# Optimization experiments

Measured on AMD Instinct MI355X. Metric: run time of the kernel, lower is better.

Reference implementation:

```python
import jax, jax.numpy as jnp
import numpy as np
from math import sqrt

D_MODEL = 1024
N_HEADS = 16
D_T = 256
D_HID = 4 * D_MODEL
EPS = 1e-6


def _rmsnorm(x):
    # RMSNorm without affine: x / sqrt(mean(x^2) + eps)
    return x * jax.lax.rsqrt(jnp.mean(x * x, axis=-1, keepdims=True) + EPS)


def setup_inputs() -> dict:
    key = jax.random.key(0)
    ks = jax.random.split(key, 16)
    s = 0.02  # weight init scale
    inp = {
        "x": jax.random.normal(ks[0], (4, 2048, D_MODEL), dtype=jnp.float32),
        "t": jax.random.normal(ks[1], (4, D_T), dtype=jnp.float32),
        # AdaRMSNorm (attn) : Linear(d_t, d_model, bias=False) weights stored (out, in)
        "attn_gamma_w": jax.random.normal(ks[2], (D_MODEL, D_T), dtype=jnp.float32) * s,
        "attn_beta_w": jax.random.normal(ks[3], (D_MODEL, D_T), dtype=jnp.float32) * s,
        # Attention projections
        "W_q": jax.random.normal(ks[4], (D_MODEL, D_MODEL), dtype=jnp.float32) * s,
        "W_k": jax.random.normal(ks[5], (D_MODEL, D_MODEL), dtype=jnp.float32) * s,
        "W_v": jax.random.normal(ks[6], (D_MODEL, D_MODEL), dtype=jnp.float32) * s,
        "W_o": jax.random.normal(ks[7], (D_MODEL, D_MODEL), dtype=jnp.float32) * s,
        "attn_alpha_w": jax.random.normal(ks[8], (D_MODEL, D_T), dtype=jnp.float32) * s,
        # AdaRMSNorm (ffn)
        "ffn_gamma_w": jax.random.normal(ks[9], (D_MODEL, D_T), dtype=jnp.float32) * s,
        "ffn_beta_w": jax.random.normal(ks[10], (D_MODEL, D_T), dtype=jnp.float32) * s,
        # SwiGLU
        "gate_w": jax.random.normal(ks[11], (D_HID, D_MODEL), dtype=jnp.float32) * s,
        "hidden_w": jax.random.normal(ks[12], (D_HID, D_MODEL), dtype=jnp.float32) * s,
        "out_w": jax.random.normal(ks[13], (D_MODEL, D_HID), dtype=jnp.float32) * s,
        "out_b": jnp.zeros((D_MODEL,), dtype=jnp.float32),
        "ffn_alpha_w": jax.random.normal(ks[14], (D_MODEL, D_T), dtype=jnp.float32) * s,
    }
    return inp


def _ada_rmsnorm(x, t, gamma_w, beta_w):
    gamma = (t @ gamma_w.T)[:, None, :]  # [b, 1, d]
    beta = (t @ beta_w.T)[:, None, :]
    return gamma * _rmsnorm(x) + beta


def _attention(x, W_q, W_k, W_v, W_o):
    b, l, dm = x.shape
    d_head = dm // N_HEADS
    scale = sqrt(N_HEADS / dm)  # == 1/sqrt(d_head)
    def split(y):  # [b, l, dm] -> [b, n, l, d]
        return y.reshape(b, l, N_HEADS, d_head).transpose(0, 2, 1, 3)
    q = split(x @ W_q.T)
    k = split(x @ W_k.T)
    v = split(x @ W_v.T)
    attn = jax.nn.softmax(scale * jnp.einsum("bnqd,bnkd->bnqk", q, k), axis=-1)
    o = jnp.einsum("bnqk,bnkd->bnqd", attn, v)
    o = o.transpose(0, 2, 1, 3).reshape(b, l, dm)
    return o @ W_o.T


def _swiglu(x, gate_w, hidden_w, out_w, out_b):
    return (jax.nn.silu(x @ gate_w.T) * (x @ hidden_w.T)) @ out_w.T + out_b


def reference(x, t, attn_gamma_w, attn_beta_w, W_q, W_k, W_v, W_o, attn_alpha_w,
              ffn_gamma_w, ffn_beta_w, gate_w, hidden_w, out_w, out_b, ffn_alpha_w):
    a_alpha = (t @ attn_alpha_w.T)[:, None, :]
    x = x + a_alpha * _attention(_ada_rmsnorm(x, t, attn_gamma_w, attn_beta_w), W_q, W_k, W_v, W_o)
    f_alpha = (t @ ffn_alpha_w.T)[:, None, :]
    return x + f_alpha * _swiglu(_ada_rmsnorm(x, t, ffn_gamma_w, ffn_beta_w), gate_w, hidden_w, out_w, out_b)
```

## Files before the change

kernel.cpp:

```cpp
#include <hip/hip_runtime.h>
#include <hip/hip_bf16.h>

typedef __attribute__((ext_vector_type(8))) short short8;
typedef __attribute__((ext_vector_type(4))) short short4v;
typedef __attribute__((ext_vector_type(4))) float f32x4;
using bf16 = __hip_bfloat16;
using lds_bf16 = __attribute__((address_space(3))) bf16;

#define BARF()  asm volatile("s_barrier" ::: "memory")
#define LGKM0() asm volatile("s_waitcnt lgkmcnt(0)" ::: "memory")
#define VMC4()  asm volatile("s_waitcnt vmcnt(4)" ::: "memory")
#define VMC0()  asm volatile("s_waitcnt vmcnt(0)" ::: "memory")
#define SCHED0() __builtin_amdgcn_sched_barrier(0)
#define PRIO1() __builtin_amdgcn_s_setprio(1)
#define PRIO0() __builtin_amdgcn_s_setprio(0)

static __device__ __forceinline__ short bfb(float f) {
  bf16 h = __float2bfloat16(f);
  short r; __builtin_memcpy(&r, &h, 2); return r;
}

static __device__ __forceinline__ void gld_lds16(const bf16* g, bf16* l) {
  __builtin_amdgcn_global_load_lds(
      (const __attribute__((address_space(1))) void*)g,
      (__attribute__((address_space(3))) void*)l, 16, 0, 0);
}

static __device__ __forceinline__ short8 dsr(const lds_bf16* b, int imm) {
  short8 v;
  asm volatile("ds_read_b128 %0, %1 offset:%2" : "=v"(v) : "v"(b), "i"(imm));
  return v;
}

__global__ __launch_bounds__(256) void cvt_all_kernel(
    const float* __restrict__ s0, const float* __restrict__ s1, const float* __restrict__ s2,
    const float* __restrict__ s3, const float* __restrict__ gw, const float* __restrict__ hw,
    const float* __restrict__ ow, bf16* __restrict__ dbase) {
  size_t c = (size_t)blockIdx.x * 256 + threadIdx.x;
  const float* src; size_t se;
  if (c < 524288) {
    int seg = (int)(c >> 17);
    src = (seg == 0) ? s0 : (seg == 1) ? s1 : (seg == 2) ? s2 : s3;
    se = (c - ((size_t)seg << 17)) * 8;
  } else if (c < 1572864) {
    size_t lc = c - 524288;
    size_t row = lc >> 7;
    src = (row & 1) ? hw : gw;
    se = ((row >> 1) << 10) + ((lc & 127) << 3);
  } else { src = ow; se = (c - 1572864) * 8; }
  float4 v0 = *(const float4*)(src + se);
  float4 v1 = *(const float4*)(src + se + 4);
  short8 o;
  o[0] = bfb(v0.x); o[1] = bfb(v0.y); o[2] = bfb(v0.z); o[3] = bfb(v0.w);
  o[4] = bfb(v1.x); o[5] = bfb(v1.y); o[6] = bfb(v1.z); o[7] = bfb(v1.w);
  *(short8*)(dbase + c * 8) = o;
}

__global__ __launch_bounds__(256) void tproj_kernel(const float* __restrict__ t,
    const float* __restrict__ w0, const float* __restrict__ w1, const float* __restrict__ w2,
    const float* __restrict__ w3, const float* __restrict__ w4, const float* __restrict__ w5,
    float* __restrict__ out) {
  int gid = blockIdx.x * 256 + threadIdx.x;
  int s = gid >> 12, rem = gid & 4095;
  int b = rem >> 10, n = rem & 1023;
  const float* w = (s == 0) ? w0 : (s == 1) ? w1 : (s == 2) ? w2 : (s == 3) ? w3 : (s == 4) ? w4 : w5;
  const float4* tv = (const float4*)(t + b * 256);
  const float4* wv = (const float4*)(w + n * 256);
  float acc = 0.f;
  #pragma unroll 8
  for (int j = 0; j < 64; ++j) {
    float4 a = tv[j], c = wv[j];
    acc += a.x * c.x + a.y * c.y + a.z * c.z + a.w * c.w;
  }
  out[gid] = acc;
}

__global__ __launch_bounds__(256) void ada_rms_kernel(const float* __restrict__ x,
    const float* __restrict__ gamma, const float* __restrict__ beta, bf16* __restrict__ out) {
  int row = blockIdx.x;
  int b = row >> 11;
  int tid = threadIdx.x;
  const float* xr = x + (size_t)row * 1024;
  float4 v = *(const float4*)(xr + tid * 4);
  float ss = v.x * v.x + v.y * v.y + v.z * v.z + v.w * v.w;
  #pragma unroll
  for (int m = 1; m < 64; m <<= 1) ss += __shfl_xor(ss, m);
  __shared__ float red[4];
  if ((tid & 63) == 0) red[tid >> 6] = ss;
  __syncthreads();
  float tot = red[0] + red[1] + red[2] + red[3];
  float rinv = rsqrtf(tot * (1.0f / 1024.0f) + 1e-6f);
  const float* g  = gamma + b * 1024 + tid * 4;
  const float* be = beta  + b * 1024 + tid * 4;
  short4v o;
  o[0] = bfb(g[0] * v.x * rinv + be[0]);
  o[1] = bfb(g[1] * v.y * rinv + be[1]);
  o[2] = bfb(g[2] * v.z * rinv + be[2]);
  o[3] = bfb(g[3] * v.w * rinv + be[3]);
  *(short4v*)(out + (size_t)row * 1024 + tid * 4) = o;
}

enum { EPI8_GH = 1 };

#define RDA_M(d, mh) { \
  _Pragma("unroll") for (int mq = 0; mq < 4; ++mq) { \
    a[mq][0] = dsr(aB0, (d) * 32768 + ((mh) * 4 + mq) * 2048); \
    a[mq][1] = dsr(aB1, (d) * 32768 + ((mh) * 4 + mq) * 2048); } }
#define RDB0_M(d, nh) { \
  _Pragma("unroll") for (int nq = 0; nq < 2; ++nq) { \
    b0[nq][0] = dsr(bB0, (d) * 32768 + ((nh) * 2 + nq) * 2048); \
    b0[nq][1] = dsr(bB1, (d) * 32768 + ((nh) * 2 + nq) * 2048); } }
#define RDB1_M(d, nh) { \
  _Pragma("unroll") for (int nq = 0; nq < 2; ++nq) { \
    b1[nq][0] = dsr(bB0, (d) * 32768 + ((nh) * 2 + nq) * 2048); \
    b1[nq][1] = dsr(bB1, (d) * 32768 + ((nh) * 2 + nq) * 2048); } }

template<int EPI>
__global__ __launch_bounds__(512, 2) void gemm8p_kernel(
    const bf16* __restrict__ A, const bf16* __restrict__ B,
    int N, int K,
    bf16* __restrict__ o1)
{
  __shared__ __align__(16) bf16 sA[2 * 2 * 128 * 64];
  __shared__ __align__(16) bf16 sB[2 * 2 * 128 * 64];
  const int tid = threadIdx.x;
  const int lane = tid & 63, w = tid >> 6;
  const int wr = w >> 2, wcn = w & 3;
  const int bid = (int)blockIdx.x;
  const int ntn = N >> 8;
  const int trow = (bid / ntn) << 8;
  const int tcol = (bid % ntn) << 8;
  const int fr = lane & 15, hi = lane >> 4;
  const int rbase = hi << 2;
  const int NITER = K >> 7;
  const int st_row = (w << 4) + (lane >> 3);
  const int st_col = (((lane & 7) ^ ((lane >> 3) & 7)) << 3);
  const bf16* AsH0 = A + (size_t)(trow + st_row) * K + st_col;
  const bf16* AsH1 = AsH0 + (size_t)128 * K;
  const bf16* BsH0 = B + (size_t)(tcol + st_row) * K + st_col;
  const bf16* BsH1 = BsH0 + (size_t)128 * K;
  const size_t K8 = (size_t)K << 3;
  bf16* dA = sA + (w << 10);
  bf16* dB = sB + (w << 10);

  auto stA = [&](int dbuf, int h, int t) {
    const bf16* s = (h ? AsH1 : AsH0) + (t << 6);
    bf16* d = dA + ((dbuf * 2 + h) << 13);
    gld_lds16(s, d);
    gld_lds16(s + K8, d + 512);
  };
  auto stB = [&](int dbuf, int h, int t) {
    const bf16* s = (h ? BsH1 : BsH0) + (t << 6);
    bf16* d = dB + ((dbuf * 2 + h) << 13);
    gld_lds16(s, d);
    gld_lds16(s + K8, d + 512);
  };
  const int colK0 = (hi << 3) ^ ((fr & 7) << 3);
  const int colK1 = (32 + (hi << 3)) ^ ((fr & 7) << 3);
  const lds_bf16* aB0 = (const lds_bf16*)(sA + (wr << 13) + (fr << 6) + colK0);
  const lds_bf16* aB1 = (const lds_bf16*)(sA + (wr << 13) + (fr << 6) + colK1);
  const lds_bf16* bB0 = (const lds_bf16*)(sB + ((wcn >> 1) << 13) + ((wcn & 1) << 12) + (fr << 6) + colK0);
  const lds_bf16* bB1 = (const lds_bf16*)(sB + ((wcn >> 1) << 13) + ((wcn & 1) << 12) + (fr << 6) + colK1);

  f32x4 acc[8][4] = {};
  short8 a[4][2], b0[2][2], b1[2][2];

  auto QUAD0 = [&](int mh, int nh) {
    #pragma unroll
    for (int kk = 0; kk < 2; ++kk)
      #pragma unroll
      for (int mq = 0; mq < 4; ++mq)
        #pragma unroll
        for (int nq = 0; nq < 2; ++nq)
          acc[mh * 4 + mq][nh * 2 + nq] = __builtin_amdgcn_mfma_f32_16x16x32_bf16(
              a[mq][kk], b0[nq][kk], acc[mh * 4 + mq][nh * 2 + nq], 0, 0, 0);
  };
  auto QUAD1 = [&](int mh, int nh) {
    #pragma unroll
    for (int kk = 0; kk < 2; ++kk)
      #pragma unroll
      for (int mq = 0; mq < 4; ++mq)
        #pragma unroll
        for (int nq = 0; nq < 2; ++nq)
          acc[mh * 4 + mq][nh * 2 + nq] = __builtin_amdgcn_mfma_f32_16x16x32_bf16(
              a[mq][kk], b1[nq][kk], acc[mh * 4 + mq][nh * 2 + nq], 0, 0, 0);
  };

  stB(0, 0, 0); stB(0, 1, 0); stA(0, 0, 0); stA(0, 1, 0);
  stB(1, 0, 1); stB(1, 1, 1);
  VMC4();
  BARF();

  for (int i = 0; i < NITER; ++i) {
    const int t1 = 2 * i + 1, tn0 = 2 * i + 2, tn1 = 2 * i + 3;
    const bool g = (i != NITER - 1);
    RDA_M(0, 0); RDB0_M(0, 0);
    stA(1, 0, t1);
    BARF(); LGKM0(); SCHED0(); PRIO1(); QUAD0(0, 0); PRIO0(); BARF();
    RDB1_M(0, 1);
    stA(1, 1, t1);
    BARF(); LGKM0(); SCHED0(); PRIO1(); QUAD1(0, 1); PRIO0(); BARF();
    RDA_M(0, 1);
    if (g) stB(0, 0, tn0);
    BARF(); LGKM0(); SCHED0(); PRIO1(); QUAD1(1, 1); PRIO0(); BARF();
    if (g) stB(0, 1, tn0);
    BARF(); LGKM0(); SCHED0(); PRIO1(); QUAD0(1, 0); PRIO0();
    if (g) { VMC4(); } else { VMC0(); }
    BARF();
    RDA_M(1, 0); RDB0_M(1, 0);
    if (g) stA(0, 0, tn0);
    BARF(); LGKM0(); SCHED0(); PRIO1(); QUAD0(0, 0); PRIO0(); BARF();
    RDB1_M(1, 1);
    if (g) stA(0, 1, tn0);
    BARF(); LGKM0(); SCHED0(); PRIO1(); QUAD1(0, 1); PRIO0(); BARF();
    RDA_M(1, 1);
    if (g) stB(1, 0, tn1);
    BARF(); LGKM0(); SCHED0(); PRIO1(); QUAD1(1, 1); PRIO0(); BARF();
    if (g) stB(1, 1, tn1);
    BARF(); LGKM0(); SCHED0(); PRIO1(); QUAD0(1, 0); PRIO0();
    if (g) { VMC4(); }
    BARF();
  }

  #pragma unroll
  for (int m = 0; m < 8; ++m)
  #pragma unroll
  for (int n = 0; n < 4; ++n)
  #pragma unroll
  for (int r = 0; r < 4; ++r) {
    int row = trow + (wr << 7) + m * 16 + rbase + r;
    int col = tcol + (wcn << 6) + n * 16 + fr;
    float c = acc[m][n][r];
    float other = __shfl_xor(c, 1);
    if (!(fr & 1)) {
      float sg = c / (1.f + __expf(-c));
      o1[(size_t)row * 4096 + (col >> 1)] = __float2bfloat16(sg * other);
    }
  }
}

enum { EPI_RESID = 0, EPI_FINAL = 1, EPI_QKV3 = 2 };

template<int EPI>
__global__ __launch_bounds__(256) void gemm_bt_kernel(
    const bf16* __restrict__ A, const bf16* __restrict__ B,
    int N, int K,
    float* __restrict__ outF,
    const float* __restrict__ aux1, const float* __restrict__ aux2,
    const float* __restrict__ bias,
    bf16* __restrict__ oq, bf16* __restrict__ okk, bf16* __restrict__ ovt)
{
  __shared__ __align__(16) bf16 As[128][32];
  __shared__ __align__(16) bf16 Bs[128][32];
  const int tid = threadIdx.x;
  const int lane = tid & 63, wid = tid >> 6;
  const int wr = wid >> 1, wc = wid & 1;
  const int bid = (int)blockIdx.x;
  const int ntn = N >> 7;
  const int trow = (bid / ntn) << 7;
  const int tcol = (bid % ntn) << 7;
  const int fr = lane & 15, fc = (lane >> 4) << 3;
  const int rbase = (lane >> 4) << 2;
  const bf16* gA0 = A + (size_t)(trow + wid * 32 + (lane >> 2)) * K + ((lane & 3) << 3);
  const bf16* gA1 = gA0 + (size_t)16 * K;
  const bf16* gB0 = B + (size_t)(tcol + wid * 32 + (lane >> 2)) * K + ((lane & 3) << 3);
  const bf16* gB1 = gB0 + (size_t)16 * K;
  bf16* lA0 = &As[wid * 32][0];
  bf16* lA1 = &As[wid * 32 + 16][0];
  bf16* lB0 = &Bs[wid * 32][0];
  bf16* lB1 = &Bs[wid * 32 + 16][0];
  f32x4 acc[4][4] = {};
  for (int k0 = 0; k0 < K; k0 += 32) {
    __syncthreads();
    gld_lds16(gA0 + k0, lA0);
    gld_lds16(gA1 + k0, lA1);
    gld_lds16(gB0 + k0, lB0);
    gld_lds16(gB1 + k0, lB1);
    __syncthreads();
    short8 af[4], bfr[4];
    #pragma unroll
    for (int m = 0; m < 4; ++m) af[m] = *(const short8*)&As[wr * 64 + m * 16 + fr][fc];
    #pragma unroll
    for (int n = 0; n < 4; ++n) bfr[n] = *(const short8*)&Bs[wc * 64 + n * 16 + fr][fc];
    #pragma unroll
    for (int m = 0; m < 4; ++m)
      #pragma unroll
      for (int n = 0; n < 4; ++n)
        acc[m][n] = __builtin_amdgcn_mfma_f32_16x16x32_bf16(af[m], bfr[n], acc[m][n], 0, 0, 0);
  }
  if constexpr (EPI == EPI_QKV3) {
    #pragma unroll
    for (int m = 0; m < 4; ++m)
    #pragma unroll
    for (int n = 0; n < 4; ++n) {
      int row0 = trow + wr * 64 + m * 16 + rbase;
      int col  = tcol + wc * 64 + n * 16 + fr;
      int seg = col >> 10, cc = col & 1023;
      int bb = row0 >> 11, h2 = cc >> 6, dd = cc & 63;
      if (seg == 0) {
        #pragma unroll
        for (int r = 0; r < 4; ++r) {
          int l = (row0 + r) & 2047;
          oq[(((size_t)(bb * 16 + h2) * 2048 + l) << 6) + dd] =
              __float2bfloat16(acc[m][n][r] * 0.18033688f);
        }
      } else if (seg == 1) {
        #pragma unroll
        for (int r = 0; r < 4; ++r) {
          int l = (row0 + r) & 2047;
          okk[(((size_t)(bb * 16 + h2) * 2048 + l) << 6) + dd] = __float2bfloat16(acc[m][n][r]);
        }
      } else {
        int l = row0 & 2047;
        short4v o4;
        #pragma unroll
        for (int r = 0; r < 4; ++r) o4[r] = bfb(acc[m][n][r]);
        *(short4v*)&ovt[(((size_t)(bb * 16 + h2) * 64 + dd) << 11) + l] = o4;
      }
    }
  } else {
    #pragma unroll
    for (int m = 0; m < 4; ++m)
    #pragma unroll
    for (int n = 0; n < 4; ++n)
    #pragma unroll
    for (int r = 0; r < 4; ++r) {
      int row = trow + wr * 64 + m * 16 + rbase + r;
      int col = tcol + wc * 64 + n * 16 + fr;
      float c = acc[m][n][r];
      int b = row >> 11;
      size_t idx = (size_t)row * 1024 + col;
      if constexpr (EPI == EPI_RESID) {
        outF[idx] = aux1[idx] + aux2[b * 1024 + col] * c;
      } else {
        outF[idx] = aux1[idx] + aux2[b * 1024 + col] * (c + bias[col]);
      }
    }
  }
}

__global__ __launch_bounds__(512, 4) void attn_kernel(const bf16* __restrict__ q,
    const bf16* __restrict__ k, const bf16* __restrict__ vt, bf16* __restrict__ o) {
  const int id = blockIdx.x;
  const int bh = id & 63;
  const int qt = id >> 6;
  const int b = bh >> 4, h = bh & 15;
  __shared__ __align__(16) bf16 Ks[2][64][72];
  __shared__ __align__(16) bf16 Vs[2][64][72];
  __shared__ __align__(16) bf16 Ps[256][72];
  const int tid = threadIdx.x, lane = tid & 63, w = tid >> 6;
  const int fr = lane & 15, hi = lane >> 4;
  const int fc = hi << 3, rbase = hi << 2;
  const bf16* qbase = q + ((size_t)bh * 2048 + qt * 256) * 64;
  const bf16* kbase = k + (size_t)bh * 2048 * 64;
  const bf16* vbase = vt + (size_t)bh * 64 * 2048;
  short8 qf[2][2];
  #pragma unroll
  for (int nq = 0; nq < 2; ++nq)
    #pragma unroll
    for (int ks = 0; ks < 2; ++ks)
      qf[nq][ks] = *(const short8*)(qbase + (size_t)(w * 32 + nq * 16 + fr) * 64 + ks * 32 + fc);
  short8 onesf;
  #pragma unroll
  for (int j = 0; j < 8; ++j) onesf[j] = (short)0x3F80;
  f32x4 accO[4][2] = {};
  f32x4 accD[2] = {};
  const int sr = tid >> 3, sc = (tid & 7) << 3;
  *(short8*)&Ks[0][sr][sc] = *(const short8*)(kbase + (size_t)sr * 64 + sc);
  *(short8*)&Vs[0][sr][sc] = *(const short8*)(vbase + (size_t)sr * 2048 + sc);
  short8 rk = *(const short8*)(kbase + (size_t)(64 + sr) * 64 + sc);
  short8 rv = *(const short8*)(vbase + (size_t)sr * 2048 + 64 + sc);
  __syncthreads();
  for (int kt = 0; kt < 2048; kt += 64) {
    const int cur = (kt >> 6) & 1;
    if (kt + 64 < 2048) {
      *(short8*)&Ks[cur ^ 1][sr][sc] = rk;
      *(short8*)&Vs[cur ^ 1][sr][sc] = rv;
      if (kt + 128 < 2048) {
        rk = *(const short8*)(kbase + (size_t)(kt + 128 + sr) * 64 + sc);
        rv = *(const short8*)(vbase + (size_t)sr * 2048 + kt + 128 + sc);
      }
    }
    f32x4 s[4][2] = {};
    #pragma unroll
    for (int ks = 0; ks < 2; ++ks) {
      short8 kf[4];
      #pragma unroll
      for (int mk = 0; mk < 4; ++mk) kf[mk] = *(const short8*)&Ks[cur][mk * 16 + fr][ks * 32 + fc];
      #pragma unroll
      for (int mk = 0; mk < 4; ++mk)
        #pragma unroll
        for (int nq = 0; nq < 2; ++nq)
          s[mk][nq] = __builtin_amdgcn_mfma_f32_16x16x32_bf16(kf[mk], qf[nq][ks], s[mk][nq], 0, 0, 0);
    }
    #pragma unroll
    for (int mk = 0; mk < 4; ++mk)
      #pragma unroll
      for (int nq = 0; nq < 2; ++nq) {
        short4v pk;
        pk[0] = bfb(exp2f(s[mk][nq][0]));
        pk[1] = bfb(exp2f(s[mk][nq][1]));
        pk[2] = bfb(exp2f(s[mk][nq][2]));
        pk[3] = bfb(exp2f(s[mk][nq][3]));
        *(short4v*)&Ps[w * 32 + nq * 16 + fr][mk * 16 + rbase] = pk;
      }
    #pragma unroll
    for (int ks2 = 0; ks2 < 2; ++ks2) {
      short8 av[4], bp[2];
      #pragma unroll
      for (int nd = 0; nd < 4; ++nd) av[nd] = *(const short8*)&Vs[cur][nd * 16 + fr][ks2 * 32 + fc];
      #pragma unroll
      for (int nq = 0; nq < 2; ++nq) bp[nq] = *(const short8*)&Ps[w * 32 + nq * 16 + fr][ks2 * 32 + fc];
      #pragma unroll
      for (int nd = 0; nd < 4; ++nd)
        #pragma unroll
        for (int nq = 0; nq < 2; ++nq)
          accO[nd][nq] = __builtin_amdgcn_mfma_f32_16x16x32_bf16(av[nd], bp[nq], accO[nd][nq], 0, 0, 0);
      #pragma unroll
      for (int nq = 0; nq < 2; ++nq)
        accD[nq] = __builtin_amdgcn_mfma_f32_16x16x32_bf16(onesf, bp[nq], accD[nq], 0, 0, 0);
    }
    __syncthreads();
  }
  float rd[2];
  #pragma unroll
  for (int nq = 0; nq < 2; ++nq) rd[nq] = 1.0f / accD[nq][0];
  #pragma unroll
  for (int nd = 0; nd < 4; ++nd)
    #pragma unroll
    for (int nq = 0; nq < 2; ++nq) {
      short4v ov;
      #pragma unroll
      for (int r = 0; r < 4; ++r) ov[r] = bfb(accO[nd][nq][r] * rd[nq]);
      int qrow = qt * 256 + w * 32 + nq * 16 + fr;
      int col = h * 64 + nd * 16 + rbase;
      *(short4v*)&o[((size_t)b * 2048 + qrow) * 1024 + col] = ov;
    }
}

extern "C" void kernel_launch(void* const* d_in, const int* in_sizes, int n_in,
                              void* d_out, int out_size, void* d_ws, size_t ws_size,
                              hipStream_t stream) {
  (void)in_sizes; (void)n_in; (void)out_size; (void)ws_size;
  const float* x   = (const float*)d_in[0];
  const float* t   = (const float*)d_in[1];
  const float* agw = (const float*)d_in[2];
  const float* abw = (const float*)d_in[3];
  const float* wq  = (const float*)d_in[4];
  const float* wk  = (const float*)d_in[5];
  const float* wv  = (const float*)d_in[6];
  const float* wo  = (const float*)d_in[7];
  const float* aaw = (const float*)d_in[8];
  const float* fgw = (const float*)d_in[9];
  const float* fbw = (const float*)d_in[10];
  const float* gw  = (const float*)d_in[11];
  const float* hw  = (const float*)d_in[12];
  const float* ow  = (const float*)d_in[13];
  const float* ob  = (const float*)d_in[14];
  const float* faw = (const float*)d_in[15];
  float* out = (float*)d_out;

  char* p = (char*)d_ws;
  auto alloc = [&](size_t bytes) -> char* {
    char* r = p; p += (bytes + 255) & ~(size_t)255; return r;
  };
  float* tp    = (float*)alloc((size_t)6 * 4096 * 4);
  bf16* wq_b   = (bf16*)alloc((size_t)1024 * 1024 * 2);
  bf16* wk_b   = (bf16*)alloc((size_t)1024 * 1024 * 2);
  bf16* wv_b   = (bf16*)alloc((size_t)1024 * 1024 * 2);
  bf16* wo_b   = (bf16*)alloc((size_t)1024 * 1024 * 2);
  bf16* wgh_b  = (bf16*)alloc((size_t)8192 * 1024 * 2);
  bf16* wout_b = (bf16*)alloc((size_t)1024 * 4096 * 2);
  bf16* xn_b   = (bf16*)alloc((size_t)8192 * 1024 * 2);
  bf16* q_b    = (bf16*)alloc((size_t)8192 * 1024 * 2);
  bf16* k_b    = (bf16*)alloc((size_t)8192 * 1024 * 2);
  bf16* vt_b   = (bf16*)alloc((size_t)8192 * 1024 * 2);
  bf16* ao_b   = (bf16*)alloc((size_t)8192 * 1024 * 2);
  float* xmid  = (float*)alloc((size_t)8192 * 1024 * 4);
  bf16* gh_b   = (bf16*)alloc((size_t)8192 * 4096 * 2);

  cvt_all_kernel<<<8192, 256, 0, stream>>>(wq, wk, wv, wo, gw, hw, ow, wq_b);
  tproj_kernel<<<96, 256, 0, stream>>>(t, agw, abw, aaw, fgw, fbw, faw, tp);
  ada_rms_kernel<<<8192, 256, 0, stream>>>(x, tp + 0 * 4096, tp + 1 * 4096, xn_b);
  gemm_bt_kernel<EPI_QKV3><<<1536, 256, 0, stream>>>(xn_b, wq_b, 3072, 1024,
      nullptr, nullptr, nullptr, nullptr, q_b, k_b, vt_b);
  attn_kernel<<<512, 512, 0, stream>>>(q_b, k_b, vt_b, ao_b);
  gemm_bt_kernel<EPI_RESID><<<512, 256, 0, stream>>>(ao_b, wo_b, 1024, 1024, xmid, x, tp + 2 * 4096, nullptr, nullptr, nullptr, nullptr);
  ada_rms_kernel<<<8192, 256, 0, stream>>>(xmid, tp + 3 * 4096, tp + 4 * 4096, xn_b);
  gemm8p_kernel<EPI8_GH><<<1024, 512, 0, stream>>>(xn_b, wgh_b, 8192, 1024, gh_b);
  gemm_bt_kernel<EPI_FINAL><<<512, 256, 0, stream>>>(gh_b, wout_b, 1024, 4096, out, xmid, tp + 5 * 4096, ob, nullptr, nullptr, nullptr);
}
```

Baseline: 558.3 us.

## Route FFN down-projection through pipelined 256x128 8-wave GEMM; reorder attention K/V staging

```diff
diff --git a/kernel.cpp b/kernel.cpp
--- a/kernel.cpp
+++ b/kernel.cpp
@@ -10,6 +10,7 @@
 #define BARF()  asm volatile("s_barrier" ::: "memory")
 #define LGKM0() asm volatile("s_waitcnt lgkmcnt(0)" ::: "memory")
 #define VMC4()  asm volatile("s_waitcnt vmcnt(4)" ::: "memory")
+#define VMC2()  asm volatile("s_waitcnt vmcnt(2)" ::: "memory")
 #define VMC0()  asm volatile("s_waitcnt vmcnt(0)" ::: "memory")
 #define SCHED0() __builtin_amdgcn_sched_barrier(0)
 #define PRIO1() __builtin_amdgcn_s_setprio(1)
@@ -100,7 +101,7 @@
   *(short4v*)(out + (size_t)row * 1024 + tid * 4) = o;
 }
 
-enum { EPI8_GH = 1 };
+enum { EPI8_GH = 1, EPI8_FIN = 2 };
 
 #define RDA_M(d, mh) { \
   _Pragma("unroll") for (int mq = 0; mq < 4; ++mq) { \
@@ -114,22 +115,27 @@
   _Pragma("unroll") for (int nq = 0; nq < 2; ++nq) { \
     b1[nq][0] = dsr(bB0, (d) * 32768 + ((nh) * 2 + nq) * 2048); \
     b1[nq][1] = dsr(bB1, (d) * 32768 + ((nh) * 2 + nq) * 2048); } }
-
-template<int EPI>
+#define RDB0_F(d) { b0[0][0] = dsr(bB0, (d) * 16384); b0[0][1] = dsr(bB1, (d) * 16384); }
+#define RDB1_F(d) { b1[0][0] = dsr(bB0, (d) * 16384 + 2048); b1[0][1] = dsr(bB1, (d) * 16384 + 2048); }
+
+template<int EPI, int BN>
 __global__ __launch_bounds__(512, 2) void gemm8p_kernel(
     const bf16* __restrict__ A, const bf16* __restrict__ B,
     int N, int K,
-    bf16* __restrict__ o1)
+    bf16* __restrict__ o1, float* __restrict__ outF,
+    const float* __restrict__ aux1, const float* __restrict__ aux2,
+    const float* __restrict__ bias)
 {
+  constexpr int SB_ELEMS = (BN == 256) ? (2 * 2 * 128 * 64) : (2 * 128 * 64);
   __shared__ __align__(16) bf16 sA[2 * 2 * 128 * 64];
-  __shared__ __align__(16) bf16 sB[2 * 2 * 128 * 64];
+  __shared__ __align__(16) bf16 sB[SB_ELEMS];
   const int tid = threadIdx.x;
   const int lane = tid & 63, w = tid >> 6;
   const int wr = w >> 2, wcn = w & 3;
   const int bid = (int)blockIdx.x;
-  const int ntn = N >> 8;
+  const int ntn = (BN == 256) ? (N >> 8) : (N >> 7);
   const int trow = (bid / ntn) << 8;
-  const int tcol = (bid % ntn) << 8;
+  const int tcol = (bid % ntn) * BN;
   const int fr = lane & 15, hi = lane >> 4;
   const int rbase = hi << 2;
   const int NITER = K >> 7;
@@ -149,9 +155,15 @@
     gld_lds16(s, d);
     gld_lds16(s + K8, d + 512);
   };
-  auto stB = [&](int dbuf, int h, int t) {
+  auto stB2 = [&](int dbuf, int h, int t) {
     const bf16* s = (h ? BsH1 : BsH0) + (t << 6);
     bf16* d = dB + ((dbuf * 2 + h) << 13);
+    gld_lds16(s, d);
+    gld_lds16(s + K8, d + 512);
+  };
+  auto stB1 = [&](int dbuf, int t) {
+    const bf16* s = BsH0 + (t << 6);
+    bf16* d = dB + (dbuf << 13);
     gld_lds16(s, d);
     gld_lds16(s + K8, d + 512);
   };
@@ -159,87 +171,147 @@
   const int colK1 = (32 + (hi << 3)) ^ ((fr & 7) << 3);
   const lds_bf16* aB0 = (const lds_bf16*)(sA + (wr << 13) + (fr << 6) + colK0);
   const lds_bf16* aB1 = (const lds_bf16*)(sA + (wr << 13) + (fr << 6) + colK1);
-  const lds_bf16* bB0 = (const lds_bf16*)(sB + ((wcn >> 1) << 13) + ((wcn & 1) << 12) + (fr << 6) + colK0);
-  const lds_bf16* bB1 = (const lds_bf16*)(sB + ((wcn >> 1) << 13) + ((wcn & 1) << 12) + (fr << 6) + colK1);
-
-  f32x4 acc[8][4] = {};
+  const lds_bf16 *bB0, *bB1;
+  if constexpr (BN == 256) {
+    bB0 = (const lds_bf16*)(sB + ((wcn >> 1) << 13) + ((wcn & 1) << 12) + (fr << 6) + colK0);
+    bB1 = (const lds_bf16*)(sB + ((wcn >> 1) << 13) + ((wcn & 1) << 12) + (fr << 6) + colK1);
+  } else {
+    bB0 = (const lds_bf16*)(sB + (wcn << 11) + (fr << 6) + colK0);
+    bB1 = (const lds_bf16*)(sB + (wcn << 11) + (fr << 6) + colK1);
+  }
+
+  f32x4 acc[8][BN / 64] = {};
   short8 a[4][2], b0[2][2], b1[2][2];
 
-  auto QUAD0 = [&](int mh, int nh) {
-    #pragma unroll
-    for (int kk = 0; kk < 2; ++kk)
-      #pragma unroll
-      for (int mq = 0; mq < 4; ++mq)
-        #pragma unroll
-        for (int nq = 0; nq < 2; ++nq)
-          acc[mh * 4 + mq][nh * 2 + nq] = __builtin_amdgcn_mfma_f32_16x16x32_bf16(
-              a[mq][kk], b0[nq][kk], acc[mh * 4 + mq][nh * 2 + nq], 0, 0, 0);
-  };
-  auto QUAD1 = [&](int mh, int nh) {
-    #pragma unroll
-    for (int kk = 0; kk < 2; ++kk)
-      #pragma unroll
-      for (int mq = 0; mq < 4; ++mq)
-        #pragma unroll
-        for (int nq = 0; nq < 2; ++nq)
-          acc[mh * 4 + mq][nh * 2 + nq] = __builtin_amdgcn_mfma_f32_16x16x32_bf16(
-              a[mq][kk], b1[nq][kk], acc[mh * 4 + mq][nh * 2 + nq], 0, 0, 0);
-  };
-
-  stB(0, 0, 0); stB(0, 1, 0); stA(0, 0, 0); stA(0, 1, 0);
-  stB(1, 0, 1); stB(1, 1, 1);
-  VMC4();
-  BARF();
-
-  for (int i = 0; i < NITER; ++i) {
-    const int t1 = 2 * i + 1, tn0 = 2 * i + 2, tn1 = 2 * i + 3;
-    const bool g = (i != NITER - 1);
-    RDA_M(0, 0); RDB0_M(0, 0);
-    stA(1, 0, t1);
-    BARF(); LGKM0(); SCHED0(); PRIO1(); QUAD0(0, 0); PRIO0(); BARF();
-    RDB1_M(0, 1);
-    stA(1, 1, t1);
-    BARF(); LGKM0(); SCHED0(); PRIO1(); QUAD1(0, 1); PRIO0(); BARF();
-    RDA_M(0, 1);
-    if (g) stB(0, 0, tn0);
-    BARF(); LGKM0(); SCHED0(); PRIO1(); QUAD1(1, 1); PRIO0(); BARF();
-    if (g) stB(0, 1, tn0);
-    BARF(); LGKM0(); SCHED0(); PRIO1(); QUAD0(1, 0); PRIO0();
-    if (g) { VMC4(); } else { VMC0(); }
+  if constexpr (BN == 256) {
+    auto QUAD0 = [&](int mh, int nh) {
+      #pragma unroll
+      for (int kk = 0; kk < 2; ++kk)
+        #pragma unroll
+        for (int mq = 0; mq < 4; ++mq)
+          #pragma unroll
+          for (int nq = 0; nq < 2; ++nq)
+            acc[mh * 4 + mq][nh * 2 + nq] = __builtin_amdgcn_mfma_f32_16x16x32_bf16(
+                a[mq][kk], b0[nq][kk], acc[mh * 4 + mq][nh * 2 + nq], 0, 0, 0);
+    };
+    auto QUAD1 = [&](int mh, int nh) {
+      #pragma unroll
+      for (int kk = 0; kk < 2; ++kk)
+        #pragma unroll
+        for (int mq = 0; mq < 4; ++mq)
+          #pragma unroll
+          for (int nq = 0; nq < 2; ++nq)
+            acc[mh * 4 + mq][nh * 2 + nq] = __builtin_amdgcn_mfma_f32_16x16x32_bf16(
+                a[mq][kk], b1[nq][kk], acc[mh * 4 + mq][nh * 2 + nq], 0, 0, 0);
+    };
+    stB2(0, 0, 0); stB2(0, 1, 0); stA(0, 0, 0); stA(0, 1, 0);
+    stB2(1, 0, 1); stB2(1, 1, 1);
+    VMC4();
     BARF();
-    RDA_M(1, 0); RDB0_M(1, 0);
-    if (g) stA(0, 0, tn0);
-    BARF(); LGKM0(); SCHED0(); PRIO1(); QUAD0(0, 0); PRIO0(); BARF();
-    RDB1_M(1, 1);
-    if (g) stA(0, 1, tn0);
-    BARF(); LGKM0(); SCHED0(); PRIO1(); QUAD1(0, 1); PRIO0(); BARF();
-    RDA_M(1, 1);
-    if (g) stB(1, 0, tn1);
-    BARF(); LGKM0(); SCHED0(); PRIO1(); QUAD1(1, 1); PRIO0(); BARF();
-    if (g) stB(1, 1, tn1);
-    BARF(); LGKM0(); SCHED0(); PRIO1(); QUAD0(1, 0); PRIO0();
-    if (g) { VMC4(); }
+    for (int i = 0; i < NITER; ++i) {
+      const int t1 = 2 * i + 1, tn0 = 2 * i + 2, tn1 = 2 * i + 3;
+      const bool g = (i != NITER - 1);
+      RDA_M(0, 0); RDB0_M(0, 0);
+      stA(1, 0, t1);
+      BARF(); LGKM0(); SCHED0(); PRIO1(); QUAD0(0, 0); PRIO0(); BARF();
+      RDB1_M(0, 1);
+      stA(1, 1, t1);
+      BARF(); LGKM0(); SCHED0(); PRIO1(); QUAD1(0, 1); PRIO0(); BARF();
+      RDA_M(0, 1);
+      if (g) stB2(0, 0, tn0);
+      BARF(); LGKM0(); SCHED0(); PRIO1(); QUAD1(1, 1); PRIO0(); BARF();
+      if (g) stB2(0, 1, tn0);
+      BARF(); LGKM0(); SCHED0(); PRIO1(); QUAD0(1, 0); PRIO0();
+      if (g) { VMC4(); } else { VMC0(); }
+      BARF();
+      RDA_M(1, 0); RDB0_M(1, 0);
+      if (g) stA(0, 0, tn0);
+      BARF(); LGKM0(); SCHED0(); PRIO1(); QUAD0(0, 0); PRIO0(); BARF();
+      RDB1_M(1, 1);
+      if (g) stA(0, 1, tn0);
+      BARF(); LGKM0(); SCHED0(); PRIO1(); QUAD1(0, 1); PRIO0(); BARF();
+      RDA_M(1, 1);
+      if (g) stB2(1, 0, tn1);
+      BARF(); LGKM0(); SCHED0(); PRIO1(); QUAD1(1, 1); PRIO0(); BARF();
+      if (g) stB2(1, 1, tn1);
+      BARF(); LGKM0(); SCHED0(); PRIO1(); QUAD0(1, 0); PRIO0();
+      if (g) { VMC4(); }
+      BARF();
+    }
+  } else {
+    auto QUADF0 = [&](int mh) {
+      #pragma unroll
+      for (int kk = 0; kk < 2; ++kk)
+        #pragma unroll
+        for (int mq = 0; mq < 4; ++mq)
+          acc[mh * 4 + mq][0] = __builtin_amdgcn_mfma_f32_16x16x32_bf16(
+              a[mq][kk], b0[0][kk], acc[mh * 4 + mq][0], 0, 0, 0);
+    };
+    auto QUADF1 = [&](int mh) {
+      #pragma unroll
+      for (int kk = 0; kk < 2; ++kk)
+        #pragma unroll
+        for (int mq = 0; mq < 4; ++mq)
+          acc[mh * 4 + mq][1] = __builtin_amdgcn_mfma_f32_16x16x32_bf16(
+              a[mq][kk], b1[0][kk], acc[mh * 4 + mq][1], 0, 0, 0);
+    };
+    stB1(0, 0); stA(0, 0, 0); stA(0, 1, 0); stB1(1, 1);
+    VMC2();
     BARF();
+    for (int i = 0; i < NITER; ++i) {
+      const int t1 = 2 * i + 1, tn0 = 2 * i + 2, tn1 = 2 * i + 3;
+      const bool g = (i != NITER - 1);
+      RDA_M(0, 0); RDB0_F(0);
+      stA(1, 0, t1);
+      BARF(); LGKM0(); SCHED0(); PRIO1(); QUADF0(0); PRIO0(); BARF();
+      RDB1_F(0);
+      stA(1, 1, t1);
+      BARF(); LGKM0(); SCHED0(); PRIO1(); QUADF1(0); PRIO0(); BARF();
+      RDA_M(0, 1);
+      if (g) stB1(0, tn0);
+      BARF(); LGKM0(); SCHED0(); PRIO1(); QUADF1(1); PRIO0(); BARF();
+      BARF(); LGKM0(); SCHED0(); PRIO1(); QUADF0(1); PRIO0();
+      if (g) { VMC2(); } else { VMC0(); }
+      BARF();
+      RDA_M(1, 0); RDB0_F(1);
+      if (g) stA(0, 0, tn0);
+      BARF(); LGKM0(); SCHED0(); PRIO1(); QUADF0(0); PRIO0(); BARF();
+      RDB1_F(1);
+      if (g) stA(0, 1, tn0);
+      BARF(); LGKM0(); SCHED0(); PRIO1(); QUADF1(0); PRIO0(); BARF();
+      RDA_M(1, 1);
+      if (g) stB1(1, tn1);
+      BARF(); LGKM0(); SCHED0(); PRIO1(); QUADF1(1); PRIO0(); BARF();
+      BARF(); LGKM0(); SCHED0(); PRIO1(); QUADF0(1); PRIO0();
+      if (g) { VMC2(); }
+      BARF();
+    }
   }
 
   #pragma unroll
   for (int m = 0; m < 8; ++m)
   #pragma unroll
-  for (int n = 0; n < 4; ++n)
+  for (int n = 0; n < BN / 64; ++n)
   #pragma unroll
   for (int r = 0; r < 4; ++r) {
     int row = trow + (wr << 7) + m * 16 + rbase + r;
-    int col = tcol + (wcn << 6) + n * 16 + fr;
+    int col = tcol + wcn * (BN / 4) + n * 16 + fr;
     float c = acc[m][n][r];
-    float other = __shfl_xor(c, 1);
-    if (!(fr & 1)) {
-      float sg = c / (1.f + __expf(-c));
-      o1[(size_t)row * 4096 + (col >> 1)] = __float2bfloat16(sg * other);
-    }
-  }
-}
-
-enum { EPI_RESID = 0, EPI_FINAL = 1, EPI_QKV3 = 2 };
+    if constexpr (EPI == EPI8_GH) {
+      float other = __shfl_xor(c, 1);
+      if (!(fr & 1)) {
+        float sg = c / (1.f + __expf(-c));
+        o1[(size_t)row * 4096 + (col >> 1)] = __float2bfloat16(sg * other);
+      }
+    } else {
+      int b = row >> 11;
+      size_t idx = (size_t)row * 1024 + col;
+      outF[idx] = aux1[idx] + aux2[b * 1024 + col] * (c + bias[col]);
+    }
+  }
+}
+
+enum { EPI_RESID = 0, EPI_QKV3 = 2 };
 
 template<int EPI>
 __global__ __launch_bounds__(256) void gemm_bt_kernel(
@@ -247,7 +319,6 @@
     int N, int K,
     float* __restrict__ outF,
     const float* __restrict__ aux1, const float* __restrict__ aux2,
-    const float* __restrict__ bias,
     bf16* __restrict__ oq, bf16* __restrict__ okk, bf16* __restrict__ ovt)
 {
   __shared__ __align__(16) bf16 As[128][32];
@@ -327,14 +398,9 @@
     for (int r = 0; r < 4; ++r) {
       int row = trow + wr * 64 + m * 16 + rbase + r;
       int col = tcol + wc * 64 + n * 16 + fr;
-      float c = acc[m][n][r];
       int b = row >> 11;
       size_t idx = (size_t)row * 1024 + col;
-      if constexpr (EPI == EPI_RESID) {
-        outF[idx] = aux1[idx] + aux2[b * 1024 + col] * c;
-      } else {
-        outF[idx] = aux1[idx] + aux2[b * 1024 + col] * (c + bias[col]);
-      }
+      outF[idx] = aux1[idx] + aux2[b * 1024 + col] * acc[m][n][r];
     }
   }
 }
@@ -373,6 +439,18 @@
   __syncthreads();
   for (int kt = 0; kt < 2048; kt += 64) {
     const int cur = (kt >> 6) & 1;
+    f32x4 s[4][2] = {};
+    #pragma unroll
+    for (int ks = 0; ks < 2; ++ks) {
+      short8 kf[4];
+      #pragma unroll
+      for (int mk = 0; mk < 4; ++mk) kf[mk] = *(const short8*)&Ks[cur][mk * 16 + fr][ks * 32 + fc];
+      #pragma unroll
+      for (int mk = 0; mk < 4; ++mk)
+        #pragma unroll
+        for (int nq = 0; nq < 2; ++nq)
+          s[mk][nq] = __builtin_amdgcn_mfma_f32_16x16x32_bf16(kf[mk], qf[nq][ks], s[mk][nq], 0, 0, 0);
+    }
     if (kt + 64 < 2048) {
       *(short8*)&Ks[cur ^ 1][sr][sc] = rk;
       *(short8*)&Vs[cur ^ 1][sr][sc] = rv;
@@ -380,18 +458,6 @@
         rk = *(const short8*)(kbase + (size_t)(kt + 128 + sr) * 64 + sc);
         rv = *(const short8*)(vbase + (size_t)sr * 2048 + kt + 128 + sc);
       }
-    }
-    f32x4 s[4][2] = {};
-    #pragma unroll
-    for (int ks = 0; ks < 2; ++ks) {
-      short8 kf[4];
-      #pragma unroll
-      for (int mk = 0; mk < 4; ++mk) kf[mk] = *(const short8*)&Ks[cur][mk * 16 + fr][ks * 32 + fc];
-      #pragma unroll
-      for (int mk = 0; mk < 4; ++mk)
-        #pragma unroll
-        for (int nq = 0; nq < 2; ++nq)
-          s[mk][nq] = __builtin_amdgcn_mfma_f32_16x16x32_bf16(kf[mk], qf[nq][ks], s[mk][nq], 0, 0, 0);
     }
     #pragma unroll
     for (int mk = 0; mk < 4; ++mk)
@@ -483,10 +549,10 @@
   tproj_kernel<<<96, 256, 0, stream>>>(t, agw, abw, aaw, fgw, fbw, faw, tp);
   ada_rms_kernel<<<8192, 256, 0, stream>>>(x, tp + 0 * 4096, tp + 1 * 4096, xn_b);
   gemm_bt_kernel<EPI_QKV3><<<1536, 256, 0, stream>>>(xn_b, wq_b, 3072, 1024,
-      nullptr, nullptr, nullptr, nullptr, q_b, k_b, vt_b);
+      nullptr, nullptr, nullptr, q_b, k_b, vt_b);
   attn_kernel<<<512, 512, 0, stream>>>(q_b, k_b, vt_b, ao_b);
-  gemm_bt_kernel<EPI_RESID><<<512, 256, 0, stream>>>(ao_b, wo_b, 1024, 1024, xmid, x, tp + 2 * 4096, nullptr, nullptr, nullptr, nullptr);
+  gemm_bt_kernel<EPI_RESID><<<512, 256, 0, stream>>>(ao_b, wo_b, 1024, 1024, xmid, x, tp + 2 * 4096, nullptr, nullptr, nullptr);
   ada_rms_kernel<<<8192, 256, 0, stream>>>(xmid, tp + 3 * 4096, tp + 4 * 4096, xn_b);
-  gemm8p_kernel<EPI8_GH><<<1024, 512, 0, stream>>>(xn_b, wgh_b, 8192, 1024, gh_b);
-  gemm_bt_kernel<EPI_FINAL><<<512, 256, 0, stream>>>(gh_b, wout_b, 1024, 4096, out, xmid, tp + 5 * 4096, ob, nullptr, nullptr, nullptr);
-}
+  gemm8p_kernel<EPI8_GH, 256><<<1024, 512, 0, stream>>>(xn_b, wgh_b, 8192, 1024, gh_b, nullptr, nullptr, nullptr, nullptr);
+  gemm8p_kernel<EPI8_FIN, 128><<<256, 512, 0, stream>>>(gh_b, wout_b, 1024, 4096, nullptr, out, xmid, tp + 5 * 4096, ob);
+}
```

After: 521.0 us, median of 2. -6.7%, faster.

## Unify all GEMMs on a pipelined 256x128-tile kernel with fused epilogues

Applied to the files above, without the earlier changes.

```diff
diff --git a/kernel.cpp b/kernel.cpp
--- a/kernel.cpp
+++ b/kernel.cpp
@@ -9,7 +9,7 @@
 
 #define BARF()  asm volatile("s_barrier" ::: "memory")
 #define LGKM0() asm volatile("s_waitcnt lgkmcnt(0)" ::: "memory")
-#define VMC4()  asm volatile("s_waitcnt vmcnt(4)" ::: "memory")
+#define VMC2()  asm volatile("s_waitcnt vmcnt(2)" ::: "memory")
 #define VMC0()  asm volatile("s_waitcnt vmcnt(0)" ::: "memory")
 #define SCHED0() __builtin_amdgcn_sched_barrier(0)
 #define PRIO1() __builtin_amdgcn_s_setprio(1)
@@ -100,36 +100,33 @@
   *(short4v*)(out + (size_t)row * 1024 + tid * 4) = o;
 }
 
-enum { EPI8_GH = 1 };
+enum { EPI8_GH = 1, EPI8_FIN = 2, EPI8_QKV = 3, EPI8_RESID = 4 };
 
 #define RDA_M(d, mh) { \
   _Pragma("unroll") for (int mq = 0; mq < 4; ++mq) { \
     a[mq][0] = dsr(aB0, (d) * 32768 + ((mh) * 4 + mq) * 2048); \
     a[mq][1] = dsr(aB1, (d) * 32768 + ((mh) * 4 + mq) * 2048); } }
-#define RDB0_M(d, nh) { \
-  _Pragma("unroll") for (int nq = 0; nq < 2; ++nq) { \
-    b0[nq][0] = dsr(bB0, (d) * 32768 + ((nh) * 2 + nq) * 2048); \
-    b0[nq][1] = dsr(bB1, (d) * 32768 + ((nh) * 2 + nq) * 2048); } }
-#define RDB1_M(d, nh) { \
-  _Pragma("unroll") for (int nq = 0; nq < 2; ++nq) { \
-    b1[nq][0] = dsr(bB0, (d) * 32768 + ((nh) * 2 + nq) * 2048); \
-    b1[nq][1] = dsr(bB1, (d) * 32768 + ((nh) * 2 + nq) * 2048); } }
+#define RDB0_F(d) { b0[0] = dsr(bB0, (d) * 16384); b0[1] = dsr(bB1, (d) * 16384); }
+#define RDB1_F(d) { b1[0] = dsr(bB0, (d) * 16384 + 2048); b1[1] = dsr(bB1, (d) * 16384 + 2048); }
 
 template<int EPI>
 __global__ __launch_bounds__(512, 2) void gemm8p_kernel(
     const bf16* __restrict__ A, const bf16* __restrict__ B,
     int N, int K,
-    bf16* __restrict__ o1)
+    bf16* __restrict__ o1, float* __restrict__ outF,
+    const float* __restrict__ aux1, const float* __restrict__ aux2,
+    const float* __restrict__ bias,
+    bf16* __restrict__ oq, bf16* __restrict__ okk, bf16* __restrict__ ovt)
 {
   __shared__ __align__(16) bf16 sA[2 * 2 * 128 * 64];
-  __shared__ __align__(16) bf16 sB[2 * 2 * 128 * 64];
+  __shared__ __align__(16) bf16 sB[2 * 128 * 64];
   const int tid = threadIdx.x;
   const int lane = tid & 63, w = tid >> 6;
   const int wr = w >> 2, wcn = w & 3;
   const int bid = (int)blockIdx.x;
-  const int ntn = N >> 8;
+  const int ntn = N >> 7;
   const int trow = (bid / ntn) << 8;
-  const int tcol = (bid % ntn) << 8;
+  const int tcol = (bid % ntn) << 7;
   const int fr = lane & 15, hi = lane >> 4;
   const int rbase = hi << 2;
   const int NITER = K >> 7;
@@ -138,7 +135,6 @@
   const bf16* AsH0 = A + (size_t)(trow + st_row) * K + st_col;
   const bf16* AsH1 = AsH0 + (size_t)128 * K;
   const bf16* BsH0 = B + (size_t)(tcol + st_row) * K + st_col;
-  const bf16* BsH1 = BsH0 + (size_t)128 * K;
   const size_t K8 = (size_t)K << 3;
   bf16* dA = sA + (w << 10);
   bf16* dB = sB + (w << 10);
@@ -149,9 +145,9 @@
     gld_lds16(s, d);
     gld_lds16(s + K8, d + 512);
   };
-  auto stB = [&](int dbuf, int h, int t) {
-    const bf16* s = (h ? BsH1 : BsH0) + (t << 6);
-    bf16* d = dB + ((dbuf * 2 + h) << 13);
+  auto stB1 = [&](int dbuf, int t) {
+    const bf16* s = BsH0 + (t << 6);
+    bf16* d = dB + (dbuf << 13);
     gld_lds16(s, d);
     gld_lds16(s + K8, d + 512);
   };
@@ -159,142 +155,69 @@
   const int colK1 = (32 + (hi << 3)) ^ ((fr & 7) << 3);
   const lds_bf16* aB0 = (const lds_bf16*)(sA + (wr << 13) + (fr << 6) + colK0);
   const lds_bf16* aB1 = (const lds_bf16*)(sA + (wr << 13) + (fr << 6) + colK1);
-  const lds_bf16* bB0 = (const lds_bf16*)(sB + ((wcn >> 1) << 13) + ((wcn & 1) << 12) + (fr << 6) + colK0);
-  const lds_bf16* bB1 = (const lds_bf16*)(sB + ((wcn >> 1) << 13) + ((wcn & 1) << 12) + (fr << 6) + colK1);
-
-  f32x4 acc[8][4] = {};
-  short8 a[4][2], b0[2][2], b1[2][2];
-
-  auto QUAD0 = [&](int mh, int nh) {
+  const lds_bf16* bB0 = (const lds_bf16*)(sB + (wcn << 11) + (fr << 6) + colK0);
+  const lds_bf16* bB1 = (const lds_bf16*)(sB + (wcn << 11) + (fr << 6) + colK1);
+
+  f32x4 acc[8][2] = {};
+  short8 a[4][2], b0[2], b1[2];
+
+  auto QUADF0 = [&](int mh) {
     #pragma unroll
     for (int kk = 0; kk < 2; ++kk)
       #pragma unroll
       for (int mq = 0; mq < 4; ++mq)
-        #pragma unroll
-        for (int nq = 0; nq < 2; ++nq)
-          acc[mh * 4 + mq][nh * 2 + nq] = __builtin_amdgcn_mfma_f32_16x16x32_bf16(
-              a[mq][kk], b0[nq][kk], acc[mh * 4 + mq][nh * 2 + nq], 0, 0, 0);
+        acc[mh * 4 + mq][0] = __builtin_amdgcn_mfma_f32_16x16x32_bf16(
+            a[mq][kk], b0[kk], acc[mh * 4 + mq][0], 0, 0, 0);
   };
-  auto QUAD1 = [&](int mh, int nh) {
+  auto QUADF1 = [&](int mh) {
     #pragma unroll
     for (int kk = 0; kk < 2; ++kk)
       #pragma unroll
       for (int mq = 0; mq < 4; ++mq)
-        #pragma unroll
-        for (int nq = 0; nq < 2; ++nq)
-          acc[mh * 4 + mq][nh * 2 + nq] = __builtin_amdgcn_mfma_f32_16x16x32_bf16(
-              a[mq][kk], b1[nq][kk], acc[mh * 4 + mq][nh * 2 + nq], 0, 0, 0);
+        acc[mh * 4 + mq][1] = __builtin_amdgcn_mfma_f32_16x16x32_bf16(
+            a[mq][kk], b1[kk], acc[mh * 4 + mq][1], 0, 0, 0);
   };
 
-  stB(0, 0, 0); stB(0, 1, 0); stA(0, 0, 0); stA(0, 1, 0);
-  stB(1, 0, 1); stB(1, 1, 1);
-  VMC4();
+  stB1(0, 0); stA(0, 0, 0); stA(0, 1, 0); stB1(1, 1);
+  VMC2();
   BARF();
 
   for (int i = 0; i < NITER; ++i) {
     const int t1 = 2 * i + 1, tn0 = 2 * i + 2, tn1 = 2 * i + 3;
     const bool g = (i != NITER - 1);
-    RDA_M(0, 0); RDB0_M(0, 0);
+    RDA_M(0, 0); RDB0_F(0);
     stA(1, 0, t1);
-    BARF(); LGKM0(); SCHED0(); PRIO1(); QUAD0(0, 0); PRIO0(); BARF();
-    RDB1_M(0, 1);
+    BARF(); LGKM0(); SCHED0(); PRIO1(); QUADF0(0); PRIO0(); BARF();
+    RDB1_F(0);
     stA(1, 1, t1);
-    BARF(); LGKM0(); SCHED0(); PRIO1(); QUAD1(0, 1); PRIO0(); BARF();
+    BARF(); LGKM0(); SCHED0(); PRIO1(); QUADF1(0); PRIO0(); BARF();
     RDA_M(0, 1);
-    if (g) stB(0, 0, tn0);
-    BARF(); LGKM0(); SCHED0(); PRIO1(); QUAD1(1, 1); PRIO0(); BARF();
-    if (g) stB(0, 1, tn0);
-    BARF(); LGKM0(); SCHED0(); PRIO1(); QUAD0(1, 0); PRIO0();
-    if (g) { VMC4(); } else { VMC0(); }
+    if (g) stB1(0, tn0);
+    BARF(); LGKM0(); SCHED0(); PRIO1(); QUADF1(1); PRIO0(); BARF();
+    BARF(); LGKM0(); SCHED0(); PRIO1(); QUADF0(1); PRIO0();
+    if (g) { VMC2(); } else { VMC0(); }
     BARF();
-    RDA_M(1, 0); RDB0_M(1, 0);
+    RDA_M(1, 0); RDB0_F(1);
     if (g) stA(0, 0, tn0);
-    BARF(); LGKM0(); SCHED0(); PRIO1(); QUAD0(0, 0); PRIO0(); BARF();
-    RDB1_M(1, 1);
+    BARF(); LGKM0(); SCHED0(); PRIO1(); QUADF0(0); PRIO0(); BARF();
+    RDB1_F(1);
     if (g) stA(0, 1, tn0);
-    BARF(); LGKM0(); SCHED0(); PRIO1(); QUAD1(0, 1); PRIO0(); BARF();
+    BARF(); LGKM0(); SCHED0(); PRIO1(); QUADF1(0); PRIO0(); BARF();
     RDA_M(1, 1);
-    if (g) stB(1, 0, tn1);
-    BARF(); LGKM0(); SCHED0(); PRIO1(); QUAD1(1, 1); PRIO0(); BARF();
-    if (g) stB(1, 1, tn1);
-    BARF(); LGKM0(); SCHED0(); PRIO1(); QUAD0(1, 0); PRIO0();
-    if (g) { VMC4(); }
+    if (g) stB1(1, tn1);
+    BARF(); LGKM0(); SCHED0(); PRIO1(); QUADF1(1); PRIO0(); BARF();
+    BARF(); LGKM0(); SCHED0(); PRIO1(); QUADF0(1); PRIO0();
+    if (g) { VMC2(); }
     BARF();
   }
 
-  #pragma unroll
-  for (int m = 0; m < 8; ++m)
-  #pragma unroll
-  for (int n = 0; n < 4; ++n)
-  #pragma unroll
-  for (int r = 0; r < 4; ++r) {
-    int row = trow + (wr << 7) + m * 16 + rbase + r;
-    int col = tcol + (wcn << 6) + n * 16 + fr;
-    float c = acc[m][n][r];
-    float other = __shfl_xor(c, 1);
-    if (!(fr & 1)) {
-      float sg = c / (1.f + __expf(-c));
-      o1[(size_t)row * 4096 + (col >> 1)] = __float2bfloat16(sg * other);
-    }
-  }
-}
-
-enum { EPI_RESID = 0, EPI_FINAL = 1, EPI_QKV3 = 2 };
-
-template<int EPI>
-__global__ __launch_bounds__(256) void gemm_bt_kernel(
-    const bf16* __restrict__ A, const bf16* __restrict__ B,
-    int N, int K,
-    float* __restrict__ outF,
-    const float* __restrict__ aux1, const float* __restrict__ aux2,
-    const float* __restrict__ bias,
-    bf16* __restrict__ oq, bf16* __restrict__ okk, bf16* __restrict__ ovt)
-{
-  __shared__ __align__(16) bf16 As[128][32];
-  __shared__ __align__(16) bf16 Bs[128][32];
-  const int tid = threadIdx.x;
-  const int lane = tid & 63, wid = tid >> 6;
-  const int wr = wid >> 1, wc = wid & 1;
-  const int bid = (int)blockIdx.x;
-  const int ntn = N >> 7;
-  const int trow = (bid / ntn) << 7;
-  const int tcol = (bid % ntn) << 7;
-  const int fr = lane & 15, fc = (lane >> 4) << 3;
-  const int rbase = (lane >> 4) << 2;
-  const bf16* gA0 = A + (size_t)(trow + wid * 32 + (lane >> 2)) * K + ((lane & 3) << 3);
-  const bf16* gA1 = gA0 + (size_t)16 * K;
-  const bf16* gB0 = B + (size_t)(tcol + wid * 32 + (lane >> 2)) * K + ((lane & 3) << 3);
-  const bf16* gB1 = gB0 + (size_t)16 * K;
-  bf16* lA0 = &As[wid * 32][0];
-  bf16* lA1 = &As[wid * 32 + 16][0];
-  bf16* lB0 = &Bs[wid * 32][0];
-  bf16* lB1 = &Bs[wid * 32 + 16][0];
-  f32x4 acc[4][4] = {};
-  for (int k0 = 0; k0 < K; k0 += 32) {
-    __syncthreads();
-    gld_lds16(gA0 + k0, lA0);
-    gld_lds16(gA1 + k0, lA1);
-    gld_lds16(gB0 + k0, lB0);
-    gld_lds16(gB1 + k0, lB1);
-    __syncthreads();
-    short8 af[4], bfr[4];
-    #pragma unroll
-    for (int m = 0; m < 4; ++m) af[m] = *(const short8*)&As[wr * 64 + m * 16 + fr][fc];
-    #pragma unroll
-    for (int n = 0; n < 4; ++n) bfr[n] = *(const short8*)&Bs[wc * 64 + n * 16 + fr][fc];
-    #pragma unroll
-    for (int m = 0; m < 4; ++m)
-      #pragma unroll
-      for (int n = 0; n < 4; ++n)
-        acc[m][n] = __builtin_amdgcn_mfma_f32_16x16x32_bf16(af[m], bfr[n], acc[m][n], 0, 0, 0);
-  }
-  if constexpr (EPI == EPI_QKV3) {
-    #pragma unroll
-    for (int m = 0; m < 4; ++m)
-    #pragma unroll
-    for (int n = 0; n < 4; ++n) {
-      int row0 = trow + wr * 64 + m * 16 + rbase;
-      int col  = tcol + wc * 64 + n * 16 + fr;
+  if constexpr (EPI == EPI8_QKV) {
+    #pragma unroll
+    for (int m = 0; m < 8; ++m)
+    #pragma unroll
+    for (int n = 0; n < 2; ++n) {
+      int row0 = trow + (wr << 7) + m * 16 + rbase;
+      int col  = tcol + wcn * 32 + n * 16 + fr;
       int seg = col >> 10, cc = col & 1023;
       int bb = row0 >> 11, h2 = cc >> 6, dd = cc & 63;
       if (seg == 0) {
@@ -320,19 +243,27 @@
     }
   } else {
     #pragma unroll
-    for (int m = 0; m < 4; ++m)
-    #pragma unroll
-    for (int n = 0; n < 4; ++n)
+    for (int m = 0; m < 8; ++m)
+    #pragma unroll
+    for (int n = 0; n < 2; ++n)
     #pragma unroll
     for (int r = 0; r < 4; ++r) {
-      int row = trow + wr * 64 + m * 16 + rbase + r;
-      int col = tcol + wc * 64 + n * 16 + fr;
+      int row = trow + (wr << 7) + m * 16 + rbase + r;
+      int col = tcol + wcn * 32 + n * 16 + fr;
       float c = acc[m][n][r];
-      int b = row >> 11;
-      size_t idx = (size_t)row * 1024 + col;
-      if constexpr (EPI == EPI_RESID) {
+      if constexpr (EPI == EPI8_GH) {
+        float other = __shfl_xor(c, 1);
+        if (!(fr & 1)) {
+          float sg = c / (1.f + __expf(-c));
+          o1[(size_t)row * 4096 + (col >> 1)] = __float2bfloat16(sg * other);
+        }
+      } else if constexpr (EPI == EPI8_RESID) {
+        int b = row >> 11;
+        size_t idx = (size_t)row * 1024 + col;
         outF[idx] = aux1[idx] + aux2[b * 1024 + col] * c;
       } else {
+        int b = row >> 11;
+        size_t idx = (size_t)row * 1024 + col;
         outF[idx] = aux1[idx] + aux2[b * 1024 + col] * (c + bias[col]);
       }
     }
@@ -373,6 +304,18 @@
   __syncthreads();
   for (int kt = 0; kt < 2048; kt += 64) {
     const int cur = (kt >> 6) & 1;
+    f32x4 s[4][2] = {};
+    #pragma unroll
+    for (int ks = 0; ks < 2; ++ks) {
+      short8 kf[4];
+      #pragma unroll
+      for (int mk = 0; mk < 4; ++mk) kf[mk] = *(const short8*)&Ks[cur][mk * 16 + fr][ks * 32 + fc];
+      #pragma unroll
+      for (int mk = 0; mk < 4; ++mk)
+        #pragma unroll
+        for (int nq = 0; nq < 2; ++nq)
+          s[mk][nq] = __builtin_amdgcn_mfma_f32_16x16x32_bf16(kf[mk], qf[nq][ks], s[mk][nq], 0, 0, 0);
+    }
     if (kt + 64 < 2048) {
       *(short8*)&Ks[cur ^ 1][sr][sc] = rk;
       *(short8*)&Vs[cur ^ 1][sr][sc] = rv;
@@ -380,18 +323,6 @@
         rk = *(const short8*)(kbase + (size_t)(kt + 128 + sr) * 64 + sc);
         rv = *(const short8*)(vbase + (size_t)sr * 2048 + kt + 128 + sc);
       }
-    }
-    f32x4 s[4][2] = {};
-    #pragma unroll
-    for (int ks = 0; ks < 2; ++ks) {
-      short8 kf[4];
-      #pragma unroll
-      for (int mk = 0; mk < 4; ++mk) kf[mk] = *(const short8*)&Ks[cur][mk * 16 + fr][ks * 32 + fc];
-      #pragma unroll
-      for (int mk = 0; mk < 4; ++mk)
-        #pragma unroll
-        for (int nq = 0; nq < 2; ++nq)
-          s[mk][nq] = __builtin_amdgcn_mfma_f32_16x16x32_bf16(kf[mk], qf[nq][ks], s[mk][nq], 0, 0, 0);
     }
     #pragma unroll
     for (int mk = 0; mk < 4; ++mk)
@@ -482,11 +413,14 @@
   cvt_all_kernel<<<8192, 256, 0, stream>>>(wq, wk, wv, wo, gw, hw, ow, wq_b);
   tproj_kernel<<<96, 256, 0, stream>>>(t, agw, abw, aaw, fgw, fbw, faw, tp);
   ada_rms_kernel<<<8192, 256, 0, stream>>>(x, tp + 0 * 4096, tp + 1 * 4096, xn_b);
-  gemm_bt_kernel<EPI_QKV3><<<1536, 256, 0, stream>>>(xn_b, wq_b, 3072, 1024,
-      nullptr, nullptr, nullptr, nullptr, q_b, k_b, vt_b);
+  gemm8p_kernel<EPI8_QKV><<<768, 512, 0, stream>>>(xn_b, wq_b, 3072, 1024,
+      nullptr, nullptr, nullptr, nullptr, nullptr, q_b, k_b, vt_b);
   attn_kernel<<<512, 512, 0, stream>>>(q_b, k_b, vt_b, ao_b);
-  gemm_bt_kernel<EPI_RESID><<<512, 256, 0, stream>>>(ao_b, wo_b, 1024, 1024, xmid, x, tp + 2 * 4096, nullptr, nullptr, nullptr, nullptr);
+  gemm8p_kernel<EPI8_RESID><<<256, 512, 0, stream>>>(ao_b, wo_b, 1024, 1024,
+      nullptr, xmid, x, tp + 2 * 4096, nullptr, nullptr, nullptr, nullptr);
   ada_rms_kernel<<<8192, 256, 0, stream>>>(xmid, tp + 3 * 4096, tp + 4 * 4096, xn_b);
-  gemm8p_kernel<EPI8_GH><<<1024, 512, 0, stream>>>(xn_b, wgh_b, 8192, 1024, gh_b);
-  gemm_bt_kernel<EPI_FINAL><<<512, 256, 0, stream>>>(gh_b, wout_b, 1024, 4096, out, xmid, tp + 5 * 4096, ob, nullptr, nullptr, nullptr);
-}
+  gemm8p_kernel<EPI8_GH><<<2048, 512, 0, stream>>>(xn_b, wgh_b, 8192, 1024,
+      gh_b, nullptr, nullptr, nullptr, nullptr, nullptr, nullptr, nullptr);
+  gemm8p_kernel<EPI8_FIN><<<256, 512, 0, stream>>>(gh_b, wout_b, 1024, 4096,
+      nullptr, out, xmid, tp + 5 * 4096, ob, nullptr, nullptr, nullptr);
+}
```

Measured after the change: 542.7 us. -2.8%, faster.
